# Performance work log

Hardware: AMD Instinct MI355X
Metric: run time of the kernel (lower is better)

## Reference

```python
import jax, jax.numpy as jnp
import numpy as np

N = 220500          # samples (5 s @ 44.1 kHz)
C = 28              # gammatone channels
L_GT = 1000         # gammatone FIR length (source default)
L_ENV = 2000        # envelope FIR length (source default)
START2POLE = 5      # Start2PoleHP -> HP applied to channels 4: (24 channels)
NGAMMA = 4          # cascaded gammatone passes
RECOMB_DB = 10.0    # Recombination_dB
EQUIV0DBSPL = 100.0 # CONFIG.equiv0dBSPL
AHR = 0.0           # CONFIG.ahr


def fir_grouped(x, h):
    """Causal per-channel FIR: y[c,n] = sum_k h[c,k] x[c,n-k]. x:[C,N], h:[C,L]."""
    L = h.shape[1]
    y = jax.lax.conv_general_dilated(
        x[None], h[:, None, ::-1], (1,), [(L - 1, 0)],
        feature_group_count=x.shape[0],
        dimension_numbers=("NCH", "OIH", "NCH"))
    return y[0]


def fir1(x, h):
    return fir_grouped(x[None, :], h[None, :])[0]


def setup_inputs() -> dict:
    key = jax.random.key(0)
    ks = jax.random.split(key, 10)
    dec_gt = jnp.exp(-jnp.arange(L_GT, dtype=jnp.float32) / 80.0)
    dec_env = jnp.exp(-jnp.arange(L_ENV, dtype=jnp.float32) / 300.0)
    x = jax.random.normal(ks[0], (N,), dtype=jnp.float32)
    gtn_imp = jax.random.normal(ks[1], (C, L_GT), dtype=jnp.float32) * 0.05 * dec_gt[None]
    hp_imp = jax.random.normal(ks[2], (C - START2POLE + 1, L_GT), dtype=jnp.float32) * 0.05 * dec_gt[None]
    chan_lpf_imp = (0.01 + 0.002 * jax.random.normal(ks[3], (C, L_ENV), dtype=jnp.float32)) * dec_env[None]
    delta256 = jnp.zeros((256,), jnp.float32).at[0].set(1.0)
    src_fwd = delta256 + 0.01 * jax.random.normal(ks[4], (256,), dtype=jnp.float32)
    src_bwd = delta256 + 0.01 * jax.random.normal(ks[5], (256,), dtype=jnp.float32)
    lpf = jnp.zeros((133,), jnp.float32).at[0].set(1.0) + 0.01 * jax.random.normal(ks[6], (133,), dtype=jnp.float32)
    expansion_ratios = 1.0 + jax.random.uniform(ks[7], (C,), dtype=jnp.float32)
    eq_loud_db = 100.0 + 10.0 * jax.random.uniform(ks[8], (C,), dtype=jnp.float32)
    delays = jax.random.randint(ks[9], (C,), 0, 200, dtype=jnp.int32)
    return {"x": x, "src_fwd": src_fwd, "src_bwd": src_bwd, "lpf": lpf,
            "gtn_imp": gtn_imp, "hp_imp": hp_imp, "chan_lpf_imp": chan_lpf_imp,
            "expansion_ratios": expansion_ratios, "eq_loud_db": eq_loud_db,
            "delays": delays}


def _cochlea(x, gtn_imp, hp_imp, chan_lpf_imp, delays, expansion_ratios, eq_loud_db, equiv_0dB_SPL):
    n = x.shape[0]
    c = gtn_imp.shape[0]
    # gammatone filterbank: NGAMMA cascaded grouped causal FIRs
    pass_n = jnp.broadcast_to(x[None, :], (c, n))
    for _ in range(NGAMMA):
        pass_n = fir_grouped(pass_n, gtn_imp)
    # per-channel delay compensation (shift left by dly, zero-fill tail)
    idx = jnp.arange(n, dtype=jnp.int32)[None, :] + delays[:, None]  # [C,N]
    gathered = jnp.take_along_axis(pass_n, jnp.minimum(idx, n - 1), axis=1)
    pass_del = jnp.where(idx < n, gathered, 0.0)
    # high-pass correction on channels Start2PoleHP-1:
    s = START2POLE - 1
    pass_del = pass_del.at[s:].set(fir_grouped(pass_del[s:], hp_imp))
    # envelope: forward-backward low-pass of rectified signal
    env_f = fir_grouped(jnp.abs(pass_del), chan_lpf_imp)
    env = fir_grouped(jnp.abs(env_f[:, ::-1]), chan_lpf_imp)[:, ::-1]
    # loudness recruitment
    envlp_max = (10.0 ** (0.05 * (eq_loud_db - equiv_0dB_SPL)))[:, None]
    env_cl = jnp.minimum(jnp.clip(env, 1e-9, None), envlp_max)
    env_norm = jnp.clip(env_cl / envlp_max, 1e-6, None)
    gain = env_norm ** (jnp.clip(expansion_ratios, -5.0, None)[:, None] - 1.0)
    gain = jnp.minimum(gain, 100.0)
    coch = pass_del * gain
    power = 10.0 ** (-0.05 * RECOMB_DB)
    return coch.sum(axis=0) * power


def reference(x, src_fwd, src_bwd, lpf, gtn_imp, hp_imp, chan_lpf_imp,
              expansion_ratios, eq_loud_db, delays):
    # level bookkeeping (as in HearingLoss.forward)
    levelreFS = 10.0 * jnp.log10(jnp.mean(x ** 2))  # noqa: F841 (calibration only)
    equiv_0dB_SPL = EQUIV0DBSPL + AHR
    # free-field -> cochlea correction
    xc = fir1(x, src_fwd)
    coch = _cochlea(xc, gtn_imp, hp_imp, chan_lpf_imp, delays,
                    expansion_ratios, eq_loud_db, equiv_0dB_SPL)
    # cochlea -> free-field correction, then 18 kHz anti-alias LPF
    out = fir1(fir1(coch, src_bwd), lpf)
    return out
```

## Files before the change

kernel.cpp:

```cpp
#include <hip/hip_runtime.h>
#include <math.h>

#define NSAMP 220500
#define NCH   28
#define HPCH  24
#define TILE  2048
#define BLOCK 256

#define LP_GT4 4032
#define L_H4F  4252
#define LP_H4F 4288
#define LP_HP  1008
#define LP_ENV 2016
#define L_TB   388
#define LP_TB  432

#define NC_GT 134
#define NC_HP 65
#define NC_EF 128
#define NC_EB 128

typedef __attribute__((ext_vector_type(4)))  float f32x4;
typedef __attribute__((ext_vector_type(16))) float f32x16;
typedef __attribute__((ext_vector_type(8)))  short bf16x8;

__device__ __forceinline__ int phys9(int u) { return u + (u >> 3); }

__device__ __forceinline__ unsigned short f2bf(float x) {
    unsigned u = __float_as_uint(x);
    u += 0x7FFFu + ((u >> 16) & 1u);
    return (unsigned short)(u >> 16);
}

#define MFMA16 __builtin_amdgcn_mfma_f32_16x16x32_bf16
#define MFMA32 __builtin_amdgcn_mfma_f32_32x32x16_bf16

__global__ void prep_frag(const float* __restrict__ taps, int pitch,
                          unsigned short* __restrict__ TF, int NC,
                          int isAsc, int split, long planeStride)
{
    const int s  = blockIdx.x;
    const int ch = blockIdx.y;
    const int l  = threadIdx.x;
    const int m  = l & 15, hib = (l >> 4) * 8;
    unsigned short* dst = TF + ((size_t)ch * NC + s) * 512 + l * 8;
#pragma unroll
    for (int i = 0; i < 8; i++) {
        int kap = hib + i;
        int k = isAsc ? (32 * s + kap - m) : (32 * s + m - 1 - kap);
        float val = (k >= 0 && k < pitch) ? taps[(size_t)ch * pitch + k] : 0.f;
        unsigned short hh = f2bf(val);
        dst[i] = hh;
        if (split) {
            float fh = __uint_as_float((unsigned)hh << 16);
            dst[planeStride + i] = f2bf(val - fh);
        }
    }
}

__global__ void prep_frag32(const float* __restrict__ taps, int pitch,
                            unsigned short* __restrict__ TF, int NC, int isAsc)
{
    const int s  = blockIdx.x;
    const int ch = blockIdx.y;
    const int l  = threadIdx.x;
    const int m  = l & 31, kb = (l >> 5) * 8;
    unsigned short* dst = TF + ((size_t)ch * NC + s) * 512 + l * 8;
#pragma unroll
    for (int i = 0; i < 8; i++) {
        int kap = kb + i;
        int k = isAsc ? (16 * s + kap - m) : (16 * s + m - 17 - kap);
        float val = (k >= 0 && k < pitch) ? taps[(size_t)ch * pitch + k] : 0.f;
        dst[i] = f2bf(val);
    }
}

__global__ __launch_bounds__(BLOCK)
void gt4_mfma4(const float* __restrict__ x, const unsigned short* __restrict__ TF,
               long plane, float* __restrict__ out)
{
    extern __shared__ float S[];
    unsigned* S32 = (unsigned*)S;
    const int jb = blockIdx.x * 2048;
    const int c0 = blockIdx.y * 4;
    const int o  = jb - 4255;
    const int DW = 3160;

    for (int v = threadIdx.x; v < DW; v += BLOCK) {
        int p0 = o + 2 * v, p1 = p0 + 1;
        float a = (p0 >= 0 && p0 < NSAMP) ? x[p0] : 0.f;
        float b = (p1 >= 0 && p1 < NSAMP) ? x[p1] : 0.f;
        S32[v + (v >> 4)] = (unsigned)f2bf(a) | ((unsigned)f2bf(b) << 16);
    }
    __syncthreads();

    const int lane = threadIdx.x & 63;
    const int w    = threadIdx.x >> 6;
    const int n    = lane & 15;
    const int hib  = lane >> 4;
    int v0 = 256 * w + 8 * n + 4 * hib + 16 * (NC_GT - 1);
    int vp = v0 + (v0 >> 4);

    const unsigned short* t0  = TF + lane * 8;
    const unsigned short* tc0 = t0 + (size_t)(c0 + 0) * NC_GT * 512;
    const unsigned short* tc1 = t0 + (size_t)(c0 + 1) * NC_GT * 512;
    const unsigned short* tc2 = t0 + (size_t)(c0 + 2) * NC_GT * 512;
    const unsigned short* tc3 = t0 + (size_t)(c0 + 3) * NC_GT * 512;

    f32x4 a00={0,0,0,0}, a01={0,0,0,0}, a10={0,0,0,0}, a11={0,0,0,0};
    f32x4 a20={0,0,0,0}, a21={0,0,0,0}, a30={0,0,0,0}, a31={0,0,0,0};

    bf16x8 h0 = *(const bf16x8*)tc0, h1 = *(const bf16x8*)tc1;
    bf16x8 h2 = *(const bf16x8*)tc2, h3 = *(const bf16x8*)tc3;
    bf16x8 l0 = *(const bf16x8*)(tc0 + plane), l1 = *(const bf16x8*)(tc1 + plane);
    bf16x8 l2 = *(const bf16x8*)(tc2 + plane), l3 = *(const bf16x8*)(tc3 + plane);

#pragma unroll 1
    for (int s = 0; s < NC_GT; ++s) {
        int sn = (s + 1 < NC_GT) ? s + 1 : s;
        size_t off = (size_t)sn * 512;
        bf16x8 nh0 = *(const bf16x8*)(tc0 + off);
        bf16x8 nh1 = *(const bf16x8*)(tc1 + off);
        bf16x8 nh2 = *(const bf16x8*)(tc2 + off);
        bf16x8 nh3 = *(const bf16x8*)(tc3 + off);
        bf16x8 nl0 = *(const bf16x8*)(tc0 + plane + off);
        bf16x8 nl1 = *(const bf16x8*)(tc1 + plane + off);
        bf16x8 nl2 = *(const bf16x8*)(tc2 + plane + off);
        bf16x8 nl3 = *(const bf16x8*)(tc3 + plane + off);

        const float* sp = S + vp;
        union U { float f[4]; bf16x8 v; } b0, b1;
        b0.f[0]=sp[0];   b0.f[1]=sp[1];   b0.f[2]=sp[2];   b0.f[3]=sp[3];
        b1.f[0]=sp[136]; b1.f[1]=sp[137]; b1.f[2]=sp[138]; b1.f[3]=sp[139];

        a00 = MFMA16(h0, b0.v, a00,0,0,0);  a00 = MFMA16(l0, b0.v, a00,0,0,0);
        a10 = MFMA16(h1, b0.v, a10,0,0,0);  a10 = MFMA16(l1, b0.v, a10,0,0,0);
        a20 = MFMA16(h2, b0.v, a20,0,0,0);  a20 = MFMA16(l2, b0.v, a20,0,0,0);
        a30 = MFMA16(h3, b0.v, a30,0,0,0);  a30 = MFMA16(l3, b0.v, a30,0,0,0);
        a01 = MFMA16(h0, b1.v, a01,0,0,0);  a01 = MFMA16(l0, b1.v, a01,0,0,0);
        a11 = MFMA16(h1, b1.v, a11,0,0,0);  a11 = MFMA16(l1, b1.v, a11,0,0,0);
        a21 = MFMA16(h2, b1.v, a21,0,0,0);  a21 = MFMA16(l2, b1.v, a21,0,0,0);
        a31 = MFMA16(h3, b1.v, a31,0,0,0);  a31 = MFMA16(l3, b1.v, a31,0,0,0);

        h0=nh0; h1=nh1; h2=nh2; h3=nh3;
        l0=nl0; l1=nl1; l2=nl2; l3=nl3;
        vp -= 17;
    }

    const int j0 = jb + 512 * w + 16 * n + 4 * hib;
    float* y0 = out + (size_t)(c0 + 0) * NSAMP;
    float* y1 = out + (size_t)(c0 + 1) * NSAMP;
    float* y2 = out + (size_t)(c0 + 2) * NSAMP;
    float* y3 = out + (size_t)(c0 + 3) * NSAMP;
    if (j0 < NSAMP) {
        *(f32x4*)(y0 + j0) = a00; *(f32x4*)(y1 + j0) = a10;
        *(f32x4*)(y2 + j0) = a20; *(f32x4*)(y3 + j0) = a30;
    }
    if (j0 + 256 < NSAMP) {
        *(f32x4*)(y0 + j0 + 256) = a01; *(f32x4*)(y1 + j0 + 256) = a11;
        *(f32x4*)(y2 + j0 + 256) = a21; *(f32x4*)(y3 + j0 + 256) = a31;
    }
}

template<int NC, bool ASC, bool ABSIN, bool DELAYED, bool GAIN>
__global__ __launch_bounds__(BLOCK)
void fir32(const float* __restrict__ in, long instride,
           const unsigned short* __restrict__ TF,
           float* __restrict__ out,
           const int* __restrict__ delays, int chan0,
           const float* __restrict__ ratios, const float* __restrict__ eqloud)
{
    extern __shared__ float S[];
    unsigned* S32 = (unsigned*)S;
    const int c  = blockIdx.y;
    const int jb = blockIdx.x * 4096;
    const float* __restrict__ xin = in + (size_t)c * instride;
    const int o = ASC ? jb : (jb + 17 - 16 * (NC - 1));
    int d = 0;
    if (DELAYED) d = delays[chan0 + c];

    const int DW = 2040 + 8 * (NC - 1);
    for (int v = threadIdx.x; v < DW; v += BLOCK) {
        int p0 = o + 2 * v, p1 = p0 + 1;
        float a = 0.f, b = 0.f;
        if (DELAYED) {
            if (p0 >= 0 && p0 + d < NSAMP) a = xin[p0 + d];
            if (p1 >= 0 && p1 + d < NSAMP) b = xin[p1 + d];
        } else {
            if (p0 >= 0 && p0 < NSAMP) a = xin[p0];
            if (p1 >= 0 && p1 < NSAMP) b = xin[p1];
        }
        if (ABSIN) { a = fabsf(a); b = fabsf(b); }
        S32[v + (v >> 4)] = (unsigned)f2bf(a) | ((unsigned)f2bf(b) << 16);
    }
    __syncthreads();

    const int lane = threadIdx.x & 63;
    const int w    = threadIdx.x >> 6;
    const int n    = lane & 31;
    const int h5   = lane >> 5;
    int v = 512 * w + 16 * n + 4 * h5 + (ASC ? 0 : 8 * (NC - 1));

    const unsigned short* tp = TF + (size_t)c * NC * 512 + lane * 8;

    f32x16 acc;
#pragma unroll
    for (int i = 0; i < 16; ++i) acc[i] = 0.f;
    bf16x8 A = *(const bf16x8*)tp;

#pragma unroll 1
    for (int s = 0; s < NC; ++s) {
        int sn = (s + 1 < NC) ? s + 1 : s;
        bf16x8 An = *(const bf16x8*)(tp + (size_t)sn * 512);
        int vp = v + (v >> 4);
        const float* sp = S + vp;
        union U { float f[4]; bf16x8 v; } B;
        B.f[0] = sp[0]; B.f[1] = sp[1]; B.f[2] = sp[2]; B.f[3] = sp[3];
        acc = MFMA32(A, B.v, acc, 0, 0, 0);
        A = An;
        v += ASC ? 8 : -8;
    }

    float* __restrict__ yo = out + (size_t)c * NSAMP;
    const int jbase = jb + 1024 * w + 32 * n + 4 * h5;
    if (!GAIN) {
#pragma unroll
        for (int g = 0; g < 4; ++g) {
            int j0 = jbase + 8 * g;
            if (j0 < NSAMP) {
                f32x4 st;
                st[0] = acc[4*g+0]; st[1] = acc[4*g+1];
                st[2] = acc[4*g+2]; st[3] = acc[4*g+3];
                *(f32x4*)(yo + j0) = st;
            }
        }
    } else {
        const float emax = exp10f(0.05f * (eqloud[c] - 100.0f));
        const float er   = fmaxf(ratios[c], -5.0f) - 1.0f;
#pragma unroll
        for (int g = 0; g < 4; ++g) {
            int j0 = jbase + 8 * g;
            if (j0 < NSAMP) {
                f32x4 pv = *(f32x4*)(yo + j0);
#pragma unroll
                for (int q = 0; q < 4; ++q) {
                    float env = acc[4*g+q];
                    float ecl = fminf(fmaxf(env, 1e-9f), emax);
                    float enr = fmaxf(ecl / emax, 1e-6f);
                    float gg  = fminf(powf(enr, er), 100.0f);
                    pv[q] *= gg;
                }
                *(f32x4*)(yo + j0) = pv;
            }
        }
    }
}

static inline size_t lds_gt4() { return (size_t)(3160 + (3160 >> 4) + 8) * 4; }
static inline size_t lds32(int NC)
{
    int DW = 2040 + 8 * (NC - 1);
    return (size_t)(DW + (DW >> 4) + 8) * 4;
}

template<bool ASC>
__device__ __forceinline__ void group8r(const float (&LO)[8], const float (&HI)[8],
                                        float (&acc)[8], const f32x4 (&T)[2])
{
#pragma unroll
    for (int kp = 0; kp < 8; kp++) {
        const float hk = T[kp >> 2][kp & 3];
#pragma unroll
        for (int j = 0; j < 8; j++) {
            const int m = ASC ? (j + kp) : (8 + j - kp);
            const float w = (m < 8) ? LO[m] : HI[m - 8];
            acc[j] = fmaf(hk, w, acc[j]);
        }
    }
}

template<int Lpad, bool DELAYED>
__global__ __launch_bounds__(BLOCK)
void fir_blk(const float* __restrict__ in, long instride,
             const float* __restrict__ taps, int tapstride,
             float* __restrict__ out, long ostride,
             const int* __restrict__ delays, int chan0)
{
    extern __shared__ float s[];
    const int c  = blockIdx.y;
    const int n0 = blockIdx.x * TILE;
    const float* __restrict__ xin = in + (long)c * instride;
    float* __restrict__ y         = out + (long)c * ostride;
    int d = 0;
    if (DELAYED) d = delays[chan0 + c];

    constexpr int E = TILE + Lpad - 1;
    for (int i = threadIdx.x; i < E; i += BLOCK) {
        int p = n0 - (Lpad - 1) + i;
        float v = 0.f;
        if (p >= 0 && p < NSAMP) {
            int q = p + d;
            if (!DELAYED || q < NSAMP) v = xin[q];
        }
        s[phys9(i + 9)] = v;
    }
    __syncthreads();

    const int t = threadIdx.x;
    constexpr int LB = Lpad / 8;
    const int B = 9 * (t + LB);
    const f32x4* tv = (const f32x4*)(taps + (long)c * tapstride);

    float Ab[8], Bb[8], Cb[8];
    float acc[8] = {0,0,0,0,0,0,0,0};
#pragma unroll
    for (int m = 0; m < 8; m++) Ab[m] = s[B + m];
#pragma unroll
    for (int m = 0; m < 8; m++) Bb[m] = s[B + 9 + m];
    f32x4 TA[2], TB[2];
    TA[0] = tv[0]; TA[1] = tv[1];

    int Mb = B - 54;
    constexpr int NIT6 = Lpad / 48;
#pragma unroll 1
    for (int im = 0; im < NIT6; ++im) {
        const float* p = s + Mb;
#pragma unroll
        for (int m = 0; m < 8; m++) Cb[m] = p[45 + m];
        TB[0] = tv[2];  TB[1] = tv[3];
        group8r<false>(Ab, Bb, acc, TA);
#pragma unroll
        for (int m = 0; m < 8; m++) Bb[m] = p[36 + m];
        TA[0] = tv[4];  TA[1] = tv[5];
        group8r<false>(Cb, Ab, acc, TB);
#pragma unroll
        for (int m = 0; m < 8; m++) Ab[m] = p[27 + m];
        TB[0] = tv[6];  TB[1] = tv[7];
        group8r<false>(Bb, Cb, acc, TA);
#pragma unroll
        for (int m = 0; m < 8; m++) Cb[m] = p[18 + m];
        TA[0] = tv[8];  TA[1] = tv[9];
        group8r<false>(Ab, Bb, acc, TB);
#pragma unroll
        for (int m = 0; m < 8; m++) Bb[m] = p[9 + m];
        TB[0] = tv[10]; TB[1] = tv[11];
        group8r<false>(Cb, Ab, acc, TA);
#pragma unroll
        for (int m = 0; m < 8; m++) Ab[m] = p[0 + m];
        TA[0] = tv[12]; TA[1] = tv[13];
        group8r<false>(Bb, Cb, acc, TB);
        Mb -= 54;
        tv += 12;
    }

    const int nb = n0 + 8 * t;
#pragma unroll
    for (int j = 0; j < 8; j++)
        if (nb + j < NSAMP) y[nb + j] = acc[j];
}

static inline size_t lds_blk(int Lpad)
{
    int umax = TILE + Lpad + 8;
    return (size_t)(umax + (umax >> 3) + 16) * 4;
}

__global__ void conv_self(const float* __restrict__ a, int astride, int La,
                          float* __restrict__ out, int ostride, int Mlen, int Mpad)
{
    extern __shared__ float s[];
    const int c = blockIdx.y;
    const float* __restrict__ ar = a + (long)c * astride;
    for (int i = threadIdx.x; i < La; i += blockDim.x) s[i] = ar[i];
    __syncthreads();
    int m = blockIdx.x * blockDim.x + threadIdx.x;
    float acc = 0.f;
    for (int k = 0; k < La; k++) {
        int mi = m - k;
        float bv = ((unsigned)mi < (unsigned)La) ? s[mi] : 0.f;
        acc = fmaf(s[k], bv, acc);
    }
    if (m < Mpad) out[(long)c * ostride + m] = (m < Mlen) ? acc : 0.f;
}

__global__ void conv_pair(const float* __restrict__ a, int astride, int La,
                          const float* __restrict__ b, int Lb,
                          float* __restrict__ out, int ostride, int Mlen, int Mpad)
{
    extern __shared__ float s[];
    const int c = blockIdx.y;
    for (int i = threadIdx.x; i < Lb; i += blockDim.x) s[i] = b[i];
    __syncthreads();
    int m = blockIdx.x * blockDim.x + threadIdx.x;
    float acc = 0.f;
    for (int k = 0; k < Lb; k++) {
        int mi = m - k;
        float av = ((unsigned)mi < (unsigned)La) ? a[(size_t)c * astride + mi] : 0.f;
        acc = fmaf(s[k], av, acc);
    }
    if (m < Mpad) out[(size_t)c * ostride + m] = (m < Mlen) ? acc : 0.f;
}

__global__ void pad_copy(const float* __restrict__ src, int L, int sstride,
                         float* __restrict__ dst, int Lpad)
{
    int c = blockIdx.y;
    int k = blockIdx.x * blockDim.x + threadIdx.x;
    if (k < Lpad) dst[(long)c * Lpad + k] = (k < L) ? src[(long)c * sstride + k] : 0.f;
}

__global__ void delay_copy(const float* __restrict__ a, float* __restrict__ b,
                           const int* __restrict__ delays)
{
    int c = blockIdx.y;
    int n = blockIdx.x * blockDim.x + threadIdx.x;
    if (n < NSAMP) {
        int q = n + delays[c];
        b[(long)c * NSAMP + n] = (q < NSAMP) ? a[(long)c * NSAMP + q] : 0.f;
    }
}

__global__ void reduce_coch(const float* __restrict__ b, float* __restrict__ coch)
{
    int n = blockIdx.x * blockDim.x + threadIdx.x;
    if (n < NSAMP) {
        float sum = 0.f;
        for (int c = 0; c < NCH; c++) sum += b[(long)c * NSAMP + n];
        coch[n] = sum * 0.31622776601683794f;
    }
}

extern "C" void kernel_launch(void* const* d_in, const int* in_sizes, int n_in,
                              void* d_out, int out_size, void* d_ws, size_t ws_size,
                              hipStream_t stream)
{
    const float* x       = (const float*)d_in[0];
    const float* src_fwd = (const float*)d_in[1];
    const float* src_bwd = (const float*)d_in[2];
    const float* lpf     = (const float*)d_in[3];
    const float* gtn     = (const float*)d_in[4];
    const float* hp      = (const float*)d_in[5];
    const float* clpf    = (const float*)d_in[6];
    const float* ratios  = (const float*)d_in[7];
    const float* eqloud  = (const float*)d_in[8];
    const int*   delays  = (const int*)d_in[9];
    float* out = (float*)d_out;

    float* ws = (float*)d_ws;
    const size_t CNs = (size_t)NCH * NSAMP;
    float* bufA  = ws;
    float* bufB  = bufA + CNs;
    float* coch  = bufB + CNs;
    float* h2    = coch + NSAMP;
    float* h4    = h2 + (size_t)NCH * 2000;
    float* h4f   = h4 + (size_t)NCH * LP_GT4;
    float* hpP   = h4f + (size_t)NCH * LP_H4F;
    float* clpfP = hpP + (size_t)HPCH * LP_HP;
    float* tb    = clpfP + (size_t)NCH * LP_ENV;

    unsigned short* TFgt = (unsigned short*)(tb + LP_TB);
    const long gtPlane = (long)NCH * NC_GT * 512;
    unsigned short* TFhp = TFgt + 2 * gtPlane;
    unsigned short* TFef = TFhp + (size_t)HPCH * NC_HP * 512;
    unsigned short* TFeb = TFef + (size_t)NCH * NC_EF * 512;

    dim3 blk(BLOCK);

    conv_self<<<dim3(8, NCH), blk, 1000 * 4, stream>>>(
        gtn, 1000, 1000, h2, 2000, 1999, 1999);
    conv_self<<<dim3(16, NCH), blk, 1999 * 4, stream>>>(
        h2, 2000, 1999, h4, LP_GT4, 3997, LP_GT4);
    conv_pair<<<dim3((LP_H4F + BLOCK - 1) / BLOCK, NCH), blk, 256 * 4, stream>>>(
        h4, LP_GT4, 3997, src_fwd, 256, h4f, LP_H4F, L_H4F, LP_H4F);
    conv_pair<<<dim3(2, 1), blk, 133 * 4, stream>>>(
        src_bwd, 0, 256, lpf, 133, tb, LP_TB, L_TB, LP_TB);
    pad_copy<<<dim3(4, HPCH), blk, 0, stream>>>(hp, 1000, 1000, hpP, LP_HP);
    pad_copy<<<dim3(8, NCH), blk, 0, stream>>>(clpf, 2000, 2000, clpfP, LP_ENV);

    prep_frag<<<dim3(NC_GT, NCH), dim3(64), 0, stream>>>(
        h4f, LP_H4F, TFgt, NC_GT, 0, 1, gtPlane);
    prep_frag32<<<dim3(NC_HP, HPCH), dim3(64), 0, stream>>>(
        hpP, LP_HP, TFhp, NC_HP, 0);
    prep_frag32<<<dim3(NC_EF, NCH), dim3(64), 0, stream>>>(
        clpfP, LP_ENV, TFef, NC_EF, 0);
    prep_frag32<<<dim3(NC_EB, NCH), dim3(64), 0, stream>>>(
        clpfP, LP_ENV, TFeb, NC_EB, 1);

    gt4_mfma4<<<dim3(108, 7), blk, lds_gt4(), stream>>>(x, TFgt, gtPlane, bufA);

    delay_copy<<<dim3((NSAMP + BLOCK - 1) / BLOCK, 4), blk, 0, stream>>>(
        bufA, bufB, delays);

    fir32<NC_HP, false, false, true, false>
        <<<dim3(54, HPCH), blk, lds32(NC_HP), stream>>>(
        bufA + 4 * (size_t)NSAMP, NSAMP, TFhp, bufB + 4 * (size_t)NSAMP,
        delays, 4, nullptr, nullptr);

    fir32<NC_EF, false, true, false, false>
        <<<dim3(54, NCH), blk, lds32(NC_EF), stream>>>(
        bufB, NSAMP, TFef, bufA, nullptr, 0, nullptr, nullptr);

    fir32<NC_EB, true, true, false, true>
        <<<dim3(54, NCH), blk, lds32(NC_EB), stream>>>(
        bufA, NSAMP, TFeb, bufB, nullptr, 0, ratios, eqloud);

    reduce_coch<<<dim3((NSAMP + BLOCK - 1) / BLOCK), blk, 0, stream>>>(bufB, coch);

    fir_blk<LP_TB, false><<<dim3(108, 1), blk, lds_blk(LP_TB), stream>>>(
        coch, 0, tb, LP_TB, out, 0, nullptr, 0);
}
```

Measured before the change: 496.5 us.

## Interleave gammatone tap fragments per group and double fir32 tile per block

Gammatone tap fragments are reordered so the four channels and both hi/lo bf16 planes of one step sit contiguously, and the LDS input layout is padded so each B operand loads as a single vector. Input fragments are software-prefetched one step ahead. The fir32 kernels now cover 8192 samples per block, with two accumulators sharing each A fragment, which halves tap-fragment reloads and block count. The trade is fewer blocks (27 per channel), so less parallelism and latency hiding, plus larger LDS and higher register pressure.

```diff
diff --git a/kernel.cpp b/kernel.cpp
--- a/kernel.cpp
+++ b/kernel.cpp
@@ -35,26 +35,23 @@
 #define MFMA16 __builtin_amdgcn_mfma_f32_16x16x32_bf16
 #define MFMA32 __builtin_amdgcn_mfma_f32_32x32x16_bf16
 
-__global__ void prep_frag(const float* __restrict__ taps, int pitch,
-                          unsigned short* __restrict__ TF, int NC,
-                          int isAsc, int split, long planeStride)
+__global__ void prep_gt(const float* __restrict__ h4f, unsigned short* __restrict__ TF2)
 {
     const int s  = blockIdx.x;
     const int ch = blockIdx.y;
+    const int g  = ch >> 2, cc = ch & 3;
     const int l  = threadIdx.x;
     const int m  = l & 15, hib = (l >> 4) * 8;
-    unsigned short* dst = TF + ((size_t)ch * NC + s) * 512 + l * 8;
+    unsigned short* base = TF2 + ((size_t)g * NC_GT + s) * 8192 + cc * 512 + l * 8;
 #pragma unroll
     for (int i = 0; i < 8; i++) {
         int kap = hib + i;
-        int k = isAsc ? (32 * s + kap - m) : (32 * s + m - 1 - kap);
-        float val = (k >= 0 && k < pitch) ? taps[(size_t)ch * pitch + k] : 0.f;
+        int k = 32 * s + m - 1 - kap;
+        float val = (k >= 0 && k < LP_H4F) ? h4f[(size_t)ch * LP_H4F + k] : 0.f;
         unsigned short hh = f2bf(val);
-        dst[i] = hh;
-        if (split) {
-            float fh = __uint_as_float((unsigned)hh << 16);
-            dst[planeStride + i] = f2bf(val - fh);
-        }
+        base[i] = hh;
+        float fh = __uint_as_float((unsigned)hh << 16);
+        base[2048 + i] = f2bf(val - fh);
     }
 }
 
@@ -75,22 +72,22 @@
     }
 }
 
+#define GTDW 3160
 __global__ __launch_bounds__(BLOCK)
-void gt4_mfma4(const float* __restrict__ x, const unsigned short* __restrict__ TF,
-               long plane, float* __restrict__ out)
+void gt4_v3(const float* __restrict__ x, const unsigned short* __restrict__ TF2,
+            float* __restrict__ out)
 {
     extern __shared__ float S[];
     unsigned* S32 = (unsigned*)S;
     const int jb = blockIdx.x * 2048;
-    const int c0 = blockIdx.y * 4;
+    const int g  = blockIdx.y;
     const int o  = jb - 4255;
-    const int DW = 3160;
-
-    for (int v = threadIdx.x; v < DW; v += BLOCK) {
+
+    for (int v = threadIdx.x; v < GTDW; v += BLOCK) {
         int p0 = o + 2 * v, p1 = p0 + 1;
         float a = (p0 >= 0 && p0 < NSAMP) ? x[p0] : 0.f;
         float b = (p1 >= 0 && p1 < NSAMP) ? x[p1] : 0.f;
-        S32[v + (v >> 4)] = (unsigned)f2bf(a) | ((unsigned)f2bf(b) << 16);
+        S32[32 + v + ((v >> 5) << 2)] = (unsigned)f2bf(a) | ((unsigned)f2bf(b) << 16);
     }
     __syncthreads();
 
@@ -98,55 +95,50 @@
     const int w    = threadIdx.x >> 6;
     const int n    = lane & 15;
     const int hib  = lane >> 4;
-    int v0 = 256 * w + 8 * n + 4 * hib + 16 * (NC_GT - 1);
-    int vp = v0 + (v0 >> 4);
-
-    const unsigned short* t0  = TF + lane * 8;
-    const unsigned short* tc0 = t0 + (size_t)(c0 + 0) * NC_GT * 512;
-    const unsigned short* tc1 = t0 + (size_t)(c0 + 1) * NC_GT * 512;
-    const unsigned short* tc2 = t0 + (size_t)(c0 + 2) * NC_GT * 512;
-    const unsigned short* tc3 = t0 + (size_t)(c0 + 3) * NC_GT * 512;
+    int v = 256 * w + 8 * n + 4 * hib + 16 * (NC_GT - 1);
+
+    const unsigned short* tpA = TF2 + (size_t)g * NC_GT * 8192 + lane * 8;
+    const unsigned short* tpB = tpA + 2048;
 
     f32x4 a00={0,0,0,0}, a01={0,0,0,0}, a10={0,0,0,0}, a11={0,0,0,0};
     f32x4 a20={0,0,0,0}, a21={0,0,0,0}, a30={0,0,0,0}, a31={0,0,0,0};
 
-    bf16x8 h0 = *(const bf16x8*)tc0, h1 = *(const bf16x8*)tc1;
-    bf16x8 h2 = *(const bf16x8*)tc2, h3 = *(const bf16x8*)tc3;
-    bf16x8 l0 = *(const bf16x8*)(tc0 + plane), l1 = *(const bf16x8*)(tc1 + plane);
-    bf16x8 l2 = *(const bf16x8*)(tc2 + plane), l3 = *(const bf16x8*)(tc3 + plane);
+    union Ub { f32x4 f; bf16x8 v; };
+    int vp = 32 + v + ((v >> 5) << 2);
+    Ub B0, B1;
+    B0.f = *(const f32x4*)(S + vp);
+    B1.f = *(const f32x4*)(S + vp + 144);
 
 #pragma unroll 1
     for (int s = 0; s < NC_GT; ++s) {
-        int sn = (s + 1 < NC_GT) ? s + 1 : s;
-        size_t off = (size_t)sn * 512;
-        bf16x8 nh0 = *(const bf16x8*)(tc0 + off);
-        bf16x8 nh1 = *(const bf16x8*)(tc1 + off);
-        bf16x8 nh2 = *(const bf16x8*)(tc2 + off);
-        bf16x8 nh3 = *(const bf16x8*)(tc3 + off);
-        bf16x8 nl0 = *(const bf16x8*)(tc0 + plane + off);
-        bf16x8 nl1 = *(const bf16x8*)(tc1 + plane + off);
-        bf16x8 nl2 = *(const bf16x8*)(tc2 + plane + off);
-        bf16x8 nl3 = *(const bf16x8*)(tc3 + plane + off);
-
-        const float* sp = S + vp;
-        union U { float f[4]; bf16x8 v; } b0, b1;
-        b0.f[0]=sp[0];   b0.f[1]=sp[1];   b0.f[2]=sp[2];   b0.f[3]=sp[3];
-        b1.f[0]=sp[136]; b1.f[1]=sp[137]; b1.f[2]=sp[138]; b1.f[3]=sp[139];
-
-        a00 = MFMA16(h0, b0.v, a00,0,0,0);  a00 = MFMA16(l0, b0.v, a00,0,0,0);
-        a10 = MFMA16(h1, b0.v, a10,0,0,0);  a10 = MFMA16(l1, b0.v, a10,0,0,0);
-        a20 = MFMA16(h2, b0.v, a20,0,0,0);  a20 = MFMA16(l2, b0.v, a20,0,0,0);
-        a30 = MFMA16(h3, b0.v, a30,0,0,0);  a30 = MFMA16(l3, b0.v, a30,0,0,0);
-        a01 = MFMA16(h0, b1.v, a01,0,0,0);  a01 = MFMA16(l0, b1.v, a01,0,0,0);
-        a11 = MFMA16(h1, b1.v, a11,0,0,0);  a11 = MFMA16(l1, b1.v, a11,0,0,0);
-        a21 = MFMA16(h2, b1.v, a21,0,0,0);  a21 = MFMA16(l2, b1.v, a21,0,0,0);
-        a31 = MFMA16(h3, b1.v, a31,0,0,0);  a31 = MFMA16(l3, b1.v, a31,0,0,0);
-
-        h0=nh0; h1=nh1; h2=nh2; h3=nh3;
-        l0=nl0; l1=nl1; l2=nl2; l3=nl3;
-        vp -= 17;
-    }
-
+        bf16x8 h0 = *(const bf16x8*)(tpA);
+        bf16x8 h1 = *(const bf16x8*)(tpA + 512);
+        bf16x8 h2 = *(const bf16x8*)(tpA + 1024);
+        bf16x8 h3 = *(const bf16x8*)(tpA + 1536);
+        bf16x8 l0 = *(const bf16x8*)(tpB);
+        bf16x8 l1 = *(const bf16x8*)(tpB + 512);
+        bf16x8 l2 = *(const bf16x8*)(tpB + 1024);
+        bf16x8 l3 = *(const bf16x8*)(tpB + 1536);
+        v -= 16;
+        vp = 32 + v + ((v >> 5) << 2);
+        Ub N0, N1;
+        N0.f = *(const f32x4*)(S + vp);
+        N1.f = *(const f32x4*)(S + vp + 144);
+
+        a00 = MFMA16(h0, B0.v, a00,0,0,0);  a00 = MFMA16(l0, B0.v, a00,0,0,0);
+        a10 = MFMA16(h1, B0.v, a10,0,0,0);  a10 = MFMA16(l1, B0.v, a10,0,0,0);
+        a20 = MFMA16(h2, B0.v, a20,0,0,0);  a20 = MFMA16(l2, B0.v, a20,0,0,0);
+        a30 = MFMA16(h3, B0.v, a30,0,0,0);  a30 = MFMA16(l3, B0.v, a30,0,0,0);
+        a01 = MFMA16(h0, B1.v, a01,0,0,0);  a01 = MFMA16(l0, B1.v, a01,0,0,0);
+        a11 = MFMA16(h1, B1.v, a11,0,0,0);  a11 = MFMA16(l1, B1.v, a11,0,0,0);
+        a21 = MFMA16(h2, B1.v, a21,0,0,0);  a21 = MFMA16(l2, B1.v, a21,0,0,0);
+        a31 = MFMA16(h3, B1.v, a31,0,0,0);  a31 = MFMA16(l3, B1.v, a31,0,0,0);
+
+        B0 = N0; B1 = N1;
+        tpA += 8192; tpB += 8192;
+    }
+
+    const int c0 = 4 * g;
     const int j0 = jb + 512 * w + 16 * n + 4 * hib;
     float* y0 = out + (size_t)(c0 + 0) * NSAMP;
     float* y1 = out + (size_t)(c0 + 1) * NSAMP;
@@ -161,25 +153,29 @@
         *(f32x4*)(y2 + j0 + 256) = a21; *(f32x4*)(y3 + j0 + 256) = a31;
     }
 }
+static inline size_t lds_gt4v3()
+{
+    return (size_t)(32 + GTDW + ((GTDW >> 5) << 2) + 16) * 4;
+}
 
 template<int NC, bool ASC, bool ABSIN, bool DELAYED, bool GAIN>
 __global__ __launch_bounds__(BLOCK)
-void fir32(const float* __restrict__ in, long instride,
-           const unsigned short* __restrict__ TF,
-           float* __restrict__ out,
-           const int* __restrict__ delays, int chan0,
-           const float* __restrict__ ratios, const float* __restrict__ eqloud)
+void fir32b(const float* __restrict__ in, long instride,
+            const unsigned short* __restrict__ TF,
+            float* __restrict__ out,
+            const int* __restrict__ delays, int chan0,
+            const float* __restrict__ ratios, const float* __restrict__ eqloud)
 {
     extern __shared__ float S[];
     unsigned* S32 = (unsigned*)S;
     const int c  = blockIdx.y;
-    const int jb = blockIdx.x * 4096;
+    const int jb = blockIdx.x * 8192;
     const float* __restrict__ xin = in + (size_t)c * instride;
     const int o = ASC ? jb : (jb + 17 - 16 * (NC - 1));
     int d = 0;
     if (DELAYED) d = delays[chan0 + c];
 
-    const int DW = 2040 + 8 * (NC - 1);
+    const int DW = 4088 + 8 * (NC - 1);
     for (int v = threadIdx.x; v < DW; v += BLOCK) {
         int p0 = o + 2 * v, p1 = p0 + 1;
         float a = 0.f, b = 0.f;
@@ -191,7 +187,7 @@
             if (p1 >= 0 && p1 < NSAMP) b = xin[p1];
         }
         if (ABSIN) { a = fabsf(a); b = fabsf(b); }
-        S32[v + (v >> 4)] = (unsigned)f2bf(a) | ((unsigned)f2bf(b) << 16);
+        S32[16 + v + (v >> 4)] = (unsigned)f2bf(a) | ((unsigned)f2bf(b) << 16);
     }
     __syncthreads();
 
@@ -199,72 +195,84 @@
     const int w    = threadIdx.x >> 6;
     const int n    = lane & 31;
     const int h5   = lane >> 5;
-    int v = 512 * w + 16 * n + 4 * h5 + (ASC ? 0 : 8 * (NC - 1));
+    int v = 1024 * w + 16 * n + 4 * h5 + (ASC ? 0 : 8 * (NC - 1));
 
     const unsigned short* tp = TF + (size_t)c * NC * 512 + lane * 8;
 
-    f32x16 acc;
-#pragma unroll
-    for (int i = 0; i < 16; ++i) acc[i] = 0.f;
+    f32x16 acc0, acc1;
+#pragma unroll
+    for (int i = 0; i < 16; ++i) { acc0[i] = 0.f; acc1[i] = 0.f; }
+
+    union Ub { float f[4]; bf16x8 v; };
     bf16x8 A = *(const bf16x8*)tp;
+    Ub b0, b1;
+    {
+        int vp = 16 + v + (v >> 4);
+        const float* sp = S + vp;
+        b0.f[0]=sp[0];   b0.f[1]=sp[1];   b0.f[2]=sp[2];   b0.f[3]=sp[3];
+        b1.f[0]=sp[544]; b1.f[1]=sp[545]; b1.f[2]=sp[546]; b1.f[3]=sp[547];
+    }
 
 #pragma unroll 1
     for (int s = 0; s < NC; ++s) {
-        int sn = (s + 1 < NC) ? s + 1 : s;
-        bf16x8 An = *(const bf16x8*)(tp + (size_t)sn * 512);
-        int vp = v + (v >> 4);
+        bf16x8 An = *(const bf16x8*)(tp + 512);
+        v += ASC ? 8 : -8;
+        int vp = 16 + v + (v >> 4);
         const float* sp = S + vp;
-        union U { float f[4]; bf16x8 v; } B;
-        B.f[0] = sp[0]; B.f[1] = sp[1]; B.f[2] = sp[2]; B.f[3] = sp[3];
-        acc = MFMA32(A, B.v, acc, 0, 0, 0);
-        A = An;
-        v += ASC ? 8 : -8;
+        Ub n0, n1;
+        n0.f[0]=sp[0];   n0.f[1]=sp[1];   n0.f[2]=sp[2];   n0.f[3]=sp[3];
+        n1.f[0]=sp[544]; n1.f[1]=sp[545]; n1.f[2]=sp[546]; n1.f[3]=sp[547];
+        acc0 = MFMA32(A, b0.v, acc0, 0, 0, 0);
+        acc1 = MFMA32(A, b1.v, acc1, 0, 0, 0);
+        A = An; b0 = n0; b1 = n1;
+        tp += 512;
     }
 
     float* __restrict__ yo = out + (size_t)c * NSAMP;
-    const int jbase = jb + 1024 * w + 32 * n + 4 * h5;
+    const int jb1 = jb + 2048 * w + 32 * n + 4 * h5;
+
     if (!GAIN) {
 #pragma unroll
         for (int g = 0; g < 4; ++g) {
-            int j0 = jbase + 8 * g;
-            if (j0 < NSAMP) {
-                f32x4 st;
-                st[0] = acc[4*g+0]; st[1] = acc[4*g+1];
-                st[2] = acc[4*g+2]; st[3] = acc[4*g+3];
-                *(f32x4*)(yo + j0) = st;
+            int ja = jb1 + 8 * g, jbx = jb1 + 1024 + 8 * g;
+            if (ja < NSAMP) {
+                f32x4 st; st[0]=acc0[4*g]; st[1]=acc0[4*g+1]; st[2]=acc0[4*g+2]; st[3]=acc0[4*g+3];
+                *(f32x4*)(yo + ja) = st;
+            }
+            if (jbx < NSAMP) {
+                f32x4 st; st[0]=acc1[4*g]; st[1]=acc1[4*g+1]; st[2]=acc1[4*g+2]; st[3]=acc1[4*g+3];
+                *(f32x4*)(yo + jbx) = st;
             }
         }
     } else {
         const float emax = exp10f(0.05f * (eqloud[c] - 100.0f));
         const float er   = fmaxf(ratios[c], -5.0f) - 1.0f;
+#define GAINST(ACC, JV) { int j0 = (JV); if (j0 < NSAMP) {                  \
+            f32x4 pv = *(f32x4*)(yo + j0);                                   \
+            _Pragma("unroll")                                                \
+            for (int q = 0; q < 4; ++q) {                                    \
+                float env = ACC[4*g+q];                                      \
+                float ecl = fminf(fmaxf(env, 1e-9f), emax);                  \
+                float enr = fmaxf(ecl / emax, 1e-6f);                        \
+                float gg  = fminf(powf(enr, er), 100.0f);                    \
+                pv[q] *= gg;                                                 \
+            }                                                                \
+            *(f32x4*)(yo + j0) = pv; } }
 #pragma unroll
         for (int g = 0; g < 4; ++g) {
-            int j0 = jbase + 8 * g;
-            if (j0 < NSAMP) {
-                f32x4 pv = *(f32x4*)(yo + j0);
-#pragma unroll
-                for (int q = 0; q < 4; ++q) {
-                    float env = acc[4*g+q];
-                    float ecl = fminf(fmaxf(env, 1e-9f), emax);
-                    float enr = fmaxf(ecl / emax, 1e-6f);
-                    float gg  = fminf(powf(enr, er), 100.0f);
-                    pv[q] *= gg;
-                }
-                *(f32x4*)(yo + j0) = pv;
-            }
+            GAINST(acc0, jb1 + 8 * g)
+            GAINST(acc1, jb1 + 1024 + 8 * g)
         }
-    }
-}
-
-static inline size_t lds_gt4() { return (size_t)(3160 + (3160 >> 4) + 8) * 4; }
-static inline size_t lds32(int NC)
-{
-    int DW = 2040 + 8 * (NC - 1);
-    return (size_t)(DW + (DW >> 4) + 8) * 4;
-}
-
-template<bool ASC>
-__device__ __forceinline__ void group8r(const float (&LO)[8], const float (&HI)[8],
+#undef GAINST
+    }
+}
+static inline size_t lds32b(int NC)
+{
+    int DW = 4088 + 8 * (NC - 1);
+    return (size_t)(16 + DW + (DW >> 4) + 32) * 4;
+}
+
+__device__ __forceinline__ void group8d(const float (&LO)[8], const float (&HI)[8],
                                         float (&acc)[8], const f32x4 (&T)[2])
 {
 #pragma unroll
@@ -272,44 +280,31 @@
         const float hk = T[kp >> 2][kp & 3];
 #pragma unroll
         for (int j = 0; j < 8; j++) {
-            const int m = ASC ? (j + kp) : (8 + j - kp);
+            const int m = 8 + j - kp;
             const float w = (m < 8) ? LO[m] : HI[m - 8];
             acc[j] = fmaf(hk, w, acc[j]);
         }
     }
 }
 
-template<int Lpad, bool DELAYED>
+template<int Lpad>
 __global__ __launch_bounds__(BLOCK)
-void fir_blk(const float* __restrict__ in, long instride,
-             const float* __restrict__ taps, int tapstride,
-             float* __restrict__ out, long ostride,
-             const int* __restrict__ delays, int chan0)
+void fir_blk(const float* __restrict__ in, const float* __restrict__ taps,
+             float* __restrict__ out)
 {
     extern __shared__ float s[];
-    const int c  = blockIdx.y;
     const int n0 = blockIdx.x * TILE;
-    const float* __restrict__ xin = in + (long)c * instride;
-    float* __restrict__ y         = out + (long)c * ostride;
-    int d = 0;
-    if (DELAYED) d = delays[chan0 + c];
-
     constexpr int E = TILE + Lpad - 1;
     for (int i = threadIdx.x; i < E; i += BLOCK) {
         int p = n0 - (Lpad - 1) + i;
-        float v = 0.f;
-        if (p >= 0 && p < NSAMP) {
-            int q = p + d;
-            if (!DELAYED || q < NSAMP) v = xin[q];
-        }
-        s[phys9(i + 9)] = v;
+        s[phys9(i + 9)] = (p >= 0 && p < NSAMP) ? in[p] : 0.f;
     }
     __syncthreads();
 
     const int t = threadIdx.x;
     constexpr int LB = Lpad / 8;
     const int B = 9 * (t + LB);
-    const f32x4* tv = (const f32x4*)(taps + (long)c * tapstride);
+    const f32x4* tv = (const f32x4*)taps;
 
     float Ab[8], Bb[8], Cb[8];
     float acc[8] = {0,0,0,0,0,0,0,0};
@@ -328,27 +323,27 @@
 #pragma unroll
         for (int m = 0; m < 8; m++) Cb[m] = p[45 + m];
         TB[0] = tv[2];  TB[1] = tv[3];
-        group8r<false>(Ab, Bb, acc, TA);
+        group8d(Ab, Bb, acc, TA);
 #pragma unroll
         for (int m = 0; m < 8; m++) Bb[m] = p[36 + m];
         TA[0] = tv[4];  TA[1] = tv[5];
-        group8r<false>(Cb, Ab, acc, TB);
+        group8d(Cb, Ab, acc, TB);
 #pragma unroll
         for (int m = 0; m < 8; m++) Ab[m] = p[27 + m];
         TB[0] = tv[6];  TB[1] = tv[7];
-        group8r<false>(Bb, Cb, acc, TA);
+        group8d(Bb, Cb, acc, TA);
 #pragma unroll
         for (int m = 0; m < 8; m++) Cb[m] = p[18 + m];
         TA[0] = tv[8];  TA[1] = tv[9];
-        group8r<false>(Ab, Bb, acc, TB);
+        group8d(Ab, Bb, acc, TB);
 #pragma unroll
         for (int m = 0; m < 8; m++) Bb[m] = p[9 + m];
         TB[0] = tv[10]; TB[1] = tv[11];
-        group8r<false>(Cb, Ab, acc, TA);
+        group8d(Cb, Ab, acc, TA);
 #pragma unroll
         for (int m = 0; m < 8; m++) Ab[m] = p[0 + m];
         TA[0] = tv[12]; TA[1] = tv[13];
-        group8r<false>(Bb, Cb, acc, TB);
+        group8d(Bb, Cb, acc, TB);
         Mb -= 54;
         tv += 12;
     }
@@ -356,9 +351,8 @@
     const int nb = n0 + 8 * t;
 #pragma unroll
     for (int j = 0; j < 8; j++)
-        if (nb + j < NSAMP) y[nb + j] = acc[j];
-}
-
+        if (nb + j < NSAMP) out[nb + j] = acc[j];
+}
 static inline size_t lds_blk(int Lpad)
 {
     int umax = TILE + Lpad + 8;
@@ -458,11 +452,10 @@
     float* clpfP = hpP + (size_t)HPCH * LP_HP;
     float* tb    = clpfP + (size_t)NCH * LP_ENV;
 
-    unsigned short* TFgt = (unsigned short*)(tb + LP_TB);
-    const long gtPlane = (long)NCH * NC_GT * 512;
-    unsigned short* TFhp = TFgt + 2 * gtPlane;
-    unsigned short* TFef = TFhp + (size_t)HPCH * NC_HP * 512;
-    unsigned short* TFeb = TFef + (size_t)NCH * NC_EF * 512;
+    unsigned short* TF2  = (unsigned short*)(tb + LP_TB);
+    unsigned short* TFhp = TF2 + (size_t)7 * NC_GT * 8192;
+    unsigned short* TFef = TFhp + (size_t)HPCH * NC_HP * 512 + 512;
+    unsigned short* TFeb = TFef + (size_t)NCH * NC_EF * 512 + 512;
 
     dim3 blk(BLOCK);
 
@@ -477,35 +470,30 @@
     pad_copy<<<dim3(4, HPCH), blk, 0, stream>>>(hp, 1000, 1000, hpP, LP_HP);
     pad_copy<<<dim3(8, NCH), blk, 0, stream>>>(clpf, 2000, 2000, clpfP, LP_ENV);
 
-    prep_frag<<<dim3(NC_GT, NCH), dim3(64), 0, stream>>>(
-        h4f, LP_H4F, TFgt, NC_GT, 0, 1, gtPlane);
-    prep_frag32<<<dim3(NC_HP, HPCH), dim3(64), 0, stream>>>(
-        hpP, LP_HP, TFhp, NC_HP, 0);
-    prep_frag32<<<dim3(NC_EF, NCH), dim3(64), 0, stream>>>(
-        clpfP, LP_ENV, TFef, NC_EF, 0);
-    prep_frag32<<<dim3(NC_EB, NCH), dim3(64), 0, stream>>>(
-        clpfP, LP_ENV, TFeb, NC_EB, 1);
-
-    gt4_mfma4<<<dim3(108, 7), blk, lds_gt4(), stream>>>(x, TFgt, gtPlane, bufA);
+    prep_gt<<<dim3(NC_GT, NCH), dim3(64), 0, stream>>>(h4f, TF2);
+    prep_frag32<<<dim3(NC_HP, HPCH), dim3(64), 0, stream>>>(hpP, LP_HP, TFhp, NC_HP, 0);
+    prep_frag32<<<dim3(NC_EF, NCH), dim3(64), 0, stream>>>(clpfP, LP_ENV, TFef, NC_EF, 0);
+    prep_frag32<<<dim3(NC_EB, NCH), dim3(64), 0, stream>>>(clpfP, LP_ENV, TFeb, NC_EB, 1);
+
+    gt4_v3<<<dim3(108, 7), blk, lds_gt4v3(), stream>>>(x, TF2, bufA);
 
     delay_copy<<<dim3((NSAMP + BLOCK - 1) / BLOCK, 4), blk, 0, stream>>>(
         bufA, bufB, delays);
 
-    fir32<NC_HP, false, false, true, false>
-        <<<dim3(54, HPCH), blk, lds32(NC_HP), stream>>>(
+    fir32b<NC_HP, false, false, true, false>
+        <<<dim3(27, HPCH), blk, lds32b(NC_HP), stream>>>(
         bufA + 4 * (size_t)NSAMP, NSAMP, TFhp, bufB + 4 * (size_t)NSAMP,
         delays, 4, nullptr, nullptr);
 
-    fir32<NC_EF, false, true, false, false>
-        <<<dim3(54, NCH), blk, lds32(NC_EF), stream>>>(
+    fir32b<NC_EF, false, true, false, false>
+        <<<dim3(27, NCH), blk, lds32b(NC_EF), stream>>>(
         bufB, NSAMP, TFef, bufA, nullptr, 0, nullptr, nullptr);
 
-    fir32<NC_EB, true, true, false, true>
-        <<<dim3(54, NCH), blk, lds32(NC_EB), stream>>>(
+    fir32b<NC_EB, true, true, false, true>
+        <<<dim3(27, NCH), blk, lds32b(NC_EB), stream>>>(
         bufA, NSAMP, TFeb, bufB, nullptr, 0, ratios, eqloud);
 
     reduce_coch<<<dim3((NSAMP + BLOCK - 1) / BLOCK), blk, 0, stream>>>(bufB, coch);
 
-    fir_blk<LP_TB, false><<<dim3(108, 1), blk, lds_blk(LP_TB), stream>>>(
-        coch, 0, tb, LP_TB, out, 0, nullptr, 0);
-}
+    fir_blk<LP_TB><<<dim3(108, 1), blk, lds_blk(LP_TB), stream>>>(coch, tb, out);
+}
```

New measurement: 520.3 us. +4.8%, slower.
